# Performance work log

Hardware: AMD Instinct MI355X
Metric: run time of the kernel (lower is better)

The kernel has to match this reference:

```python
import jax, jax.numpy as jnp
import numpy as np

B, T_MEL, T_TXT = 16, 2048, 1024
D_MODEL, D_ENC_M, D_ENC_T = 512, 512, 512
LN_EPS = 1e-5


def setup_inputs() -> dict:
    key = jax.random.key(0)
    ks = jax.random.split(key, 9)
    mel_encoding = jax.random.normal(ks[0], (B, T_MEL, D_ENC_M), dtype=jnp.float32)
    text_encoding = jax.random.normal(ks[1], (B, T_TXT, D_ENC_T), dtype=jnp.float32)
    mel_mask = jax.random.randint(ks[2], (B, T_MEL), 0, 2).astype(bool)
    mel_mask = mel_mask.at[:, 0].set(False)  # guarantee >=1 unmasked key per row
    src_mask = jax.random.randint(ks[3], (B, T_TXT), 0, 2).astype(bool)
    # Projection weights stored [in, out] (torch Linear does x @ W.T)
    sc = 1.0 / np.sqrt(D_ENC_M)
    Wq = jax.random.uniform(ks[4], (D_ENC_T, D_MODEL), jnp.float32, -sc, sc)
    Wk = jax.random.uniform(ks[5], (D_ENC_M, D_MODEL), jnp.float32, -sc, sc)
    Wv = jax.random.uniform(ks[6], (D_ENC_M, D_MODEL), jnp.float32, -sc, sc)
    ln_gamma = jnp.ones((D_MODEL,), jnp.float32)
    ln_beta = jnp.zeros((D_MODEL,), jnp.float32)
    return {"mel_encoding": mel_encoding, "text_encoding": text_encoding,
            "mel_mask": mel_mask, "src_mask": src_mask,
            "Wq": Wq, "Wk": Wk, "Wv": Wv,
            "ln_gamma": ln_gamma, "ln_beta": ln_beta}


def reference(mel_encoding, text_encoding, mel_mask, src_mask, Wq, Wk, Wv, ln_gamma, ln_beta):
    temperature = jnp.sqrt(jnp.float32(D_ENC_M))
    q = jnp.einsum('btd,dm->btm', text_encoding, Wq)   # [B, T_txt, d_model]
    k = jnp.einsum('bsd,dm->bsm', mel_encoding, Wk)    # [B, T_mel, d_model]
    v = jnp.einsum('bsd,dm->bsm', mel_encoding, Wv)
    # attn_mask = outer product of src_mask and mel_mask (True -> masked)
    attn_mask = src_mask[:, :, None] & mel_mask[:, None, :]  # [B, T_txt, T_mel]
    scores = jnp.einsum('btm,bsm->bts', q, k) / temperature
    scores = jnp.where(attn_mask, -jnp.inf, scores)
    attn = jax.nn.softmax(scores, axis=2)
    output = jnp.einsum('bts,bsm->btm', attn, v)
    # dropout is identity at inference; LayerNorm over last dim
    mean = jnp.mean(output, axis=-1, keepdims=True)
    var = jnp.var(output, axis=-1, keepdims=True)
    output = (output - mean) * jax.lax.rsqrt(var + LN_EPS) * ln_gamma + ln_beta
    return output, attn
```

## Files before the change

kernel.cpp:

```cpp
#include <hip/hip_runtime.h>

#define DEV __device__ __forceinline__

typedef __attribute__((ext_vector_type(8))) short short8v;
typedef __attribute__((ext_vector_type(4))) float f32x4;

DEV unsigned short f2bf(float f) {
  unsigned int x = __float_as_uint(f);
  x = x + 0x7FFFu + ((x >> 16) & 1u);
  return (unsigned short)(x >> 16);
}
DEV float bf2f(unsigned short u) {
  return __uint_as_float(((unsigned)u) << 16);
}

DEV int swz_byte(int row, int kElem) {
  int chunk = ((kElem >> 3) ^ (row & 7));
  return row * 128 + (chunk << 4) + ((kElem & 7) << 1);
}

template <int ROUNDS>
DEV void stage(const unsigned short* __restrict__ g, int ld,
               unsigned short* tile, int tid) {
  const int wave = tid >> 6, l = tid & 63;
#pragma unroll
  for (int p = 0; p < ROUNDS; ++p) {
    const int r = (p << 5) + (wave << 3) + (l >> 3);
    const int c = ((l & 7) ^ (r & 7)) << 3;
    const unsigned short* src = g + (long)r * ld + c;
#if __has_builtin(__builtin_amdgcn_global_load_lds)
    unsigned short* dst = tile + (p << 11) + (wave << 9);
    __builtin_amdgcn_global_load_lds(
        (const __attribute__((address_space(1))) void*)src,
        (__attribute__((address_space(3))) void*)dst, 16, 0, 0);
#else
    short8v v = *reinterpret_cast<const short8v*>(src);
    *reinterpret_cast<short8v*>(reinterpret_cast<char*>(tile) +
                                (p << 12) + (wave << 10) + (l << 4)) = v;
#endif
  }
}

template <int BM>
DEV void stage_f32(const float* __restrict__ g, int ld,
                   unsigned short* tile, int tid) {
  const int rl = tid >> 4;
  const int c4 = (tid & 15) << 2;
#pragma unroll
  for (int p = 0; p < BM / 16; ++p) {
    const int row = (p << 4) + rl;
    const float4 f = *reinterpret_cast<const float4*>(g + (long)row * ld + c4);
    ushort4 pack;
    pack.x = f2bf(f.x); pack.y = f2bf(f.y); pack.z = f2bf(f.z); pack.w = f2bf(f.w);
    *reinterpret_cast<ushort4*>(reinterpret_cast<char*>(tile) +
                                swz_byte(row, c4)) = pack;
  }
}

template <int BM, int EPI, int GM, bool AF32>
__global__ __launch_bounds__(256) void gemm_bf16(
    const void* __restrict__ Av, const unsigned short* __restrict__ B,
    void* __restrict__ Cout, int M, int N, int K,
    long aBatch, long bBatch, long cBatch,
    const int* __restrict__ srcMask, const int* __restrict__ melMask,
    float scale, float* __restrict__ stats) {
  constexpr int NI = BM / 32;
  __shared__ unsigned short As[BM * 64];
  __shared__ unsigned short Bs[128 * 64];
  const int tid = threadIdx.x;
  const int lane = tid & 63;
  const int wave = tid >> 6;
  int z, bmi, bni;
  if constexpr (GM == 1) {
    const int id = blockIdx.x;
    z = (id & 7) | ((id >> 10) << 3);
    const int ib = (id >> 3) & 127;
    bni = ib & 15;
    bmi = ib >> 4;
  } else if constexpr (GM == 2) {
    bmi = blockIdx.x; bni = blockIdx.y; z = blockIdx.z;
  } else {
    bni = blockIdx.x; bmi = blockIdx.y; z = blockIdx.z;
  }
  const int bm = bmi * BM;
  const int bn = bni * 128;
  const unsigned short* Bb = B + (long)z * bBatch;
  const long cOff = (long)z * cBatch;
  const int wr = (wave >> 1) * (BM / 2);
  const int wc = (wave & 1) * 64;
  const int l15 = lane & 15;
  const int lHi = lane >> 4;

  f32x4 acc[NI][4] = {};

  for (int kt = 0; kt < K; kt += 64) {
    if constexpr (AF32) {
      stage_f32<BM>((const float*)Av + (long)z * aBatch + (long)bm * K + kt, K, As, tid);
    } else {
      stage<BM / 32>((const unsigned short*)Av + (long)z * aBatch + (long)bm * K + kt,
                     K, As, tid);
    }
    stage<4>(Bb + (long)bn * K + kt, K, Bs, tid);
    __syncthreads();
#pragma unroll
    for (int ks = 0; ks < 2; ++ks) {
      const int k0 = (ks << 5) + (lHi << 3);
      short8v af[NI], bfr[4];
#pragma unroll
      for (int i = 0; i < NI; ++i)
        af[i] = *reinterpret_cast<const short8v*>(
            reinterpret_cast<const char*>(As) + swz_byte(wr + i * 16 + l15, k0));
#pragma unroll
      for (int j = 0; j < 4; ++j)
        bfr[j] = *reinterpret_cast<const short8v*>(
            reinterpret_cast<const char*>(Bs) + swz_byte(wc + j * 16 + l15, k0));
#pragma unroll
      for (int i = 0; i < NI; ++i)
#pragma unroll
        for (int j = 0; j < 4; ++j)
          acc[i][j] = __builtin_amdgcn_mfma_f32_16x16x32_bf16(af[i], bfr[j], acc[i][j], 0, 0, 0);
    }
    __syncthreads();
  }

  if constexpr (EPI == 2) {
    const int wcIdx = wave & 1;
#pragma unroll
    for (int i = 0; i < NI; ++i) {
#pragma unroll
      for (int rr = 0; rr < 4; ++rr) {
        const int rloc = wr + i * 16 + lHi * 4 + rr;
        const int rb = bm + rloc;
        const bool sm = srcMask[z * 1024 + rb] != 0;
        float vals[4];
        float m_l = -3.0e38f;
#pragma unroll
        for (int j = 0; j < 4; ++j) {
          const int c = bn + wc + j * 16 + l15;
          const bool mm = melMask[z * 2048 + c] != 0;
          const float vf = (sm && mm) ? -1e30f : acc[i][j][rr] * scale;
          vals[j] = vf;
          m_l = fmaxf(m_l, vf);
        }
#pragma unroll
        for (int o = 1; o < 16; o <<= 1) m_l = fmaxf(m_l, __shfl_xor(m_l, o, 64));
        float s_l = 0.f;
#pragma unroll
        for (int j = 0; j < 4; ++j) {
          const float pe = __expf(vals[j] - m_l);
          s_l += pe;
          const int c = bn + wc + j * 16 + l15;
          reinterpret_cast<unsigned short*>(Cout)[cOff + (long)rb * N + c] = f2bf(pe);
        }
#pragma unroll
        for (int o = 1; o < 16; o <<= 1) s_l += __shfl_xor(s_l, o, 64);
        if (l15 == 0) {
          const long sidx = ((long)(z * 1024 + rb)) * 64 + (long)(bni * 2 + wcIdx) * 2;
          stats[sidx] = m_l;
          stats[sidx + 1] = s_l;
        }
      }
    }
  } else {
#pragma unroll
    for (int i = 0; i < NI; ++i) {
#pragma unroll
      for (int j = 0; j < 4; ++j) {
        const int rb = bm + wr + i * 16 + lHi * 4;
        const int c = bn + wc + j * 16 + l15;
#pragma unroll
        for (int r = 0; r < 4; ++r) {
          const long idx = cOff + (long)(rb + r) * N + c;
          reinterpret_cast<unsigned short*>(Cout)[idx] = f2bf(acc[i][j][r]);
        }
      }
    }
  }
}

__global__ __launch_bounds__(256) void pv_smx(
    const unsigned short* __restrict__ sbf, const unsigned short* __restrict__ vT,
    float* __restrict__ attn, float* __restrict__ out,
    const float* __restrict__ stats) {
  __shared__ unsigned short As[2][64 * 64];
  __shared__ unsigned short Bs[2][128 * 64];
  __shared__ unsigned short scl[64][34];
  const int id = blockIdx.x;
  const int z = (id & 7) | ((id >> 9) << 3);
  const int ib = (id >> 3) & 63;
  const int mt = ib & 15, nt = ib >> 4;
  const int bm = mt * 64, bn = nt * 128;
  const int tid = threadIdx.x, lane = tid & 63, wave = tid >> 6;

  {
    const int row = tid >> 2;
    const float* st = stats + ((long)(z * 1024 + bm + row)) * 64;
    float Mx = -3.0e38f;
#pragma unroll
    for (int t = 0; t < 32; ++t) Mx = fmaxf(Mx, st[t * 2]);
    float S = 0.f;
#pragma unroll
    for (int t = 0; t < 32; ++t) S += st[t * 2 + 1] * __expf(st[t * 2] - Mx);
    const float inv = 1.0f / S;
    const int t0 = (tid & 3) * 8;
#pragma unroll
    for (int t = 0; t < 8; ++t)
      scl[row][t0 + t] = f2bf(__expf(st[(t0 + t) * 2] - Mx) * inv);
  }
  __syncthreads();

  const int ar = tid >> 2;
  const int ac = (tid & 3) << 4;
  const long aOff = ((long)z * 1024 + bm + ar) * 2048 + ac;
  const unsigned short* vTb = vT + ((long)z * 512 + bn) * 2048;
  const int wr = (wave >> 1) * 32, wc = (wave & 1) * 64;
  const int l15 = lane & 15, lHi = lane >> 4;

  f32x4 acc[2][4] = {};

  for (int it = 0; it < 16; ++it) {
    const int kt = it << 7;
    stage<4>(vTb + kt, 2048, Bs[0], tid);
    stage<4>(vTb + kt + 64, 2048, Bs[1], tid);
#pragma unroll
    for (int h = 0; h < 2; ++h) {
      const int kh = kt + (h << 6);
      const float sc = bf2f(scl[ar][kh >> 6]);
      const short8v s0 = *reinterpret_cast<const short8v*>(sbf + aOff + kh);
      const short8v s1 = *reinterpret_cast<const short8v*>(sbf + aOff + kh + 8);
      float e[16];
#pragma unroll
      for (int u = 0; u < 8; ++u) {
        e[u] = bf2f((unsigned short)s0[u]) * sc;
        e[u + 8] = bf2f((unsigned short)s1[u]) * sc;
      }
      if ((kh >> 9) == nt) {
        float* ap = attn + aOff + kh;
#pragma unroll
        for (int g = 0; g < 4; ++g) {
          float4 w;
          w.x = e[g * 4]; w.y = e[g * 4 + 1]; w.z = e[g * 4 + 2]; w.w = e[g * 4 + 3];
          *reinterpret_cast<float4*>(ap + g * 4) = w;
        }
      }
      short8v pk0, pk1;
#pragma unroll
      for (int u = 0; u < 8; ++u) {
        pk0[u] = (short)f2bf(e[u]);
        pk1[u] = (short)f2bf(e[u + 8]);
      }
      *reinterpret_cast<short8v*>(reinterpret_cast<char*>(As[h]) + swz_byte(ar, ac)) = pk0;
      *reinterpret_cast<short8v*>(reinterpret_cast<char*>(As[h]) + swz_byte(ar, ac + 8)) = pk1;
    }
    __syncthreads();

#pragma unroll
    for (int h = 0; h < 2; ++h) {
#pragma unroll
      for (int ks = 0; ks < 2; ++ks) {
        const int k0 = (ks << 5) + (lHi << 3);
        short8v af[2], bfr[4];
#pragma unroll
        for (int i = 0; i < 2; ++i)
          af[i] = *reinterpret_cast<const short8v*>(
              reinterpret_cast<const char*>(As[h]) + swz_byte(wr + i * 16 + l15, k0));
#pragma unroll
        for (int j = 0; j < 4; ++j)
          bfr[j] = *reinterpret_cast<const short8v*>(
              reinterpret_cast<const char*>(Bs[h]) + swz_byte(wc + j * 16 + l15, k0));
#pragma unroll
        for (int i = 0; i < 2; ++i)
#pragma unroll
          for (int j = 0; j < 4; ++j)
            acc[i][j] = __builtin_amdgcn_mfma_f32_16x16x32_bf16(af[i], bfr[j], acc[i][j], 0, 0, 0);
      }
    }
    __syncthreads();
  }

#pragma unroll
  for (int i = 0; i < 2; ++i)
#pragma unroll
    for (int j = 0; j < 4; ++j) {
      const int row = bm + wr + i * 16 + lHi * 4;
      const int col = bn + wc + j * 16 + l15;
#pragma unroll
      for (int rr = 0; rr < 4; ++rr)
        out[((long)z * 1024 + row + rr) * 512 + col] = acc[i][j][rr];
    }
}

__global__ __launch_bounds__(256) void f32_to_bf16(
    const float* __restrict__ in, unsigned short* __restrict__ out, long n) {
  long i = ((long)blockIdx.x * blockDim.x + threadIdx.x) * 8;
  const long stride = (long)gridDim.x * blockDim.x * 8;
  for (; i < n; i += stride) {
    const float4 a = *reinterpret_cast<const float4*>(in + i);
    const float4 b = *reinterpret_cast<const float4*>(in + i + 4);
    short8v o;
    o[0] = (short)f2bf(a.x); o[1] = (short)f2bf(a.y);
    o[2] = (short)f2bf(a.z); o[3] = (short)f2bf(a.w);
    o[4] = (short)f2bf(b.x); o[5] = (short)f2bf(b.y);
    o[6] = (short)f2bf(b.z); o[7] = (short)f2bf(b.w);
    *reinterpret_cast<short8v*>(out + i) = o;
  }
}

__global__ __launch_bounds__(256) void prep_w(
    const float* __restrict__ Wq, const float* __restrict__ Wk,
    const float* __restrict__ Wv, unsigned short* __restrict__ wqbf,
    unsigned short* __restrict__ wkbf, unsigned short* __restrict__ WvT) {
  const int zz = blockIdx.z;
  const int tx = threadIdx.x, ty = threadIdx.y;
  if (zz == 0) {
    __shared__ float t[32][33];
    const int bx = blockIdx.x * 32;
    const int by = blockIdx.y * 32;
#pragma unroll
    for (int i = 0; i < 4; ++i)
      t[ty + i * 8][tx] = Wv[(long)(by + ty + i * 8) * 512 + bx + tx];
    __syncthreads();
#pragma unroll
    for (int i = 0; i < 4; ++i)
      WvT[(long)(bx + ty + i * 8) * 512 + by + tx] = f2bf(t[tx][ty + i * 8]);
  } else {
    const float* in = (zz == 1) ? Wq : Wk;
    unsigned short* out = (zz == 1) ? wqbf : wkbf;
    const long base = ((long)(blockIdx.y * 16 + blockIdx.x) * 256 + ty * 32 + tx) * 4;
    const float4 f = *reinterpret_cast<const float4*>(in + base);
    ushort4 o;
    o.x = f2bf(f.x); o.y = f2bf(f.y); o.z = f2bf(f.z); o.w = f2bf(f.w);
    *reinterpret_cast<ushort4*>(out + base) = o;
  }
}

__global__ __launch_bounds__(64) void layernorm_rows(
    float* __restrict__ out, const float* __restrict__ gamma, const float* __restrict__ beta) {
  const long row = blockIdx.x;
  float4* p = reinterpret_cast<float4*>(out + row * 512);
  const int lane = threadIdx.x;
  float4 a = p[lane];
  float4 b = p[lane + 64];
  float s = ((a.x + a.y) + (a.z + a.w)) + ((b.x + b.y) + (b.z + b.w));
  float s2 = ((a.x * a.x + a.y * a.y) + (a.z * a.z + a.w * a.w)) +
             ((b.x * b.x + b.y * b.y) + (b.z * b.z + b.w * b.w));
#pragma unroll
  for (int o = 32; o; o >>= 1) {
    s += __shfl_xor(s, o, 64);
    s2 += __shfl_xor(s2, o, 64);
  }
  const float mean = s * (1.0f / 512.0f);
  const float var = s2 * (1.0f / 512.0f) - mean * mean;
  const float rstd = rsqrtf(var + 1e-5f);
  const float4 g0 = reinterpret_cast<const float4*>(gamma)[lane];
  const float4 g1 = reinterpret_cast<const float4*>(gamma)[lane + 64];
  const float4 c0 = reinterpret_cast<const float4*>(beta)[lane];
  const float4 c1 = reinterpret_cast<const float4*>(beta)[lane + 64];
  a.x = (a.x - mean) * rstd * g0.x + c0.x;
  a.y = (a.y - mean) * rstd * g0.y + c0.y;
  a.z = (a.z - mean) * rstd * g0.z + c0.z;
  a.w = (a.w - mean) * rstd * g0.w + c0.w;
  b.x = (b.x - mean) * rstd * g1.x + c1.x;
  b.y = (b.y - mean) * rstd * g1.y + c1.y;
  b.z = (b.z - mean) * rstd * g1.z + c1.z;
  b.w = (b.w - mean) * rstd * g1.w + c1.w;
  p[lane] = a;
  p[lane + 64] = b;
}

extern "C" void kernel_launch(void* const* d_in, const int* in_sizes, int n_in,
                              void* d_out, int out_size, void* d_ws, size_t ws_size,
                              hipStream_t stream) {
  const float* mel  = (const float*)d_in[0];
  const float* text = (const float*)d_in[1];
  const int* melMask = (const int*)d_in[2];
  const int* srcMask = (const int*)d_in[3];
  const float* Wq = (const float*)d_in[4];
  const float* Wk = (const float*)d_in[5];
  const float* Wv = (const float*)d_in[6];
  const float* gamma = (const float*)d_in[7];
  const float* beta  = (const float*)d_in[8];

  float* out = (float*)d_out;
  float* attn = (float*)d_out + (long)16 * 1024 * 512;

  unsigned short* ws = (unsigned short*)d_ws;
  unsigned short* wqbf = ws;
  unsigned short* wkbf = wqbf + 512 * 512;
  unsigned short* wvT  = wkbf + 512 * 512;
  unsigned short* Mt   = wvT + 512 * 512;
  unsigned short* melbf = Mt + 512 * 512;
  unsigned short* qbf  = melbf + (long)16 * 2048 * 512;
  unsigned short* vT   = qbf + (long)16 * 1024 * 512;
  unsigned short* sbf  = vT + (long)16 * 512 * 2048;
  float* stats = (float*)(sbf + (long)16 * 1024 * 2048);

  prep_w<<<dim3(16, 16, 3), dim3(32, 8), 0, stream>>>(Wq, Wk, Wv, wqbf, wkbf, wvT);
  f32_to_bf16<<<dim3(4096), 256, 0, stream>>>(mel, melbf, (long)16 * 2048 * 512);

  gemm_bf16<128, 0, 0, false><<<dim3(4, 4, 1), 256, 0, stream>>>(
      wkbf, wqbf, Mt, 512, 512, 512, 0, 0, 0, nullptr, nullptr, 1.0f, nullptr);
  gemm_bf16<128, 0, 2, true><<<dim3(128, 4, 1), 256, 0, stream>>>(
      text, Mt, qbf, 16384, 512, 512, 0, 0, 0, nullptr, nullptr, 1.0f, nullptr);
  gemm_bf16<128, 0, 0, false><<<dim3(16, 4, 16), 256, 0, stream>>>(
      wvT, melbf, vT, 512, 2048, 512, 0, (long)2048 * 512, (long)512 * 2048,
      nullptr, nullptr, 1.0f, nullptr);
  gemm_bf16<128, 2, 1, false><<<dim3(2048), 256, 0, stream>>>(
      qbf, melbf, sbf, 1024, 2048, 512,
      (long)1024 * 512, (long)2048 * 512, (long)1024 * 2048,
      srcMask, melMask, 0.044194173824159216f, stats);
  pv_smx<<<dim3(1024), 256, 0, stream>>>(sbf, vT, attn, out, stats);
  layernorm_rows<<<dim3(16 * 1024), 64, 0, stream>>>(out, gamma, beta);
}
```

Measured before the change: 260.8 us.

## Merge independent launches into interleaved horizontally fused kernels

Moves the GEMM body into a device function and builds two combined kernels. One pairs the mel f32-to-bf16 conversion with the Q projection GEMM, and the other pairs the V-transpose GEMM with the scores GEMM, splitting block IDs by a fixed ratio. The aim is to save launch gaps and let memory-bound and compute-bound work share the GPU at the same time. The cost is that both halves of each combined kernel must use the same shared-memory size and register budget.

```diff
diff --git a/kernel.cpp b/kernel.cpp
--- a/kernel.cpp
+++ b/kernel.cpp
@@ -57,31 +57,18 @@
   }
 }
 
-template <int BM, int EPI, int GM, bool AF32>
-__global__ __launch_bounds__(256) void gemm_bf16(
-    const void* __restrict__ Av, const unsigned short* __restrict__ B,
-    void* __restrict__ Cout, int M, int N, int K,
-    long aBatch, long bBatch, long cBatch,
-    const int* __restrict__ srcMask, const int* __restrict__ melMask,
-    float scale, float* __restrict__ stats) {
+template <int BM, int EPI, bool AF32>
+DEV void gemm_body(const void* __restrict__ Av, const unsigned short* __restrict__ B,
+                   void* __restrict__ Cout, int M, int N, int K,
+                   long aBatch, long bBatch, long cBatch,
+                   const int* __restrict__ srcMask, const int* __restrict__ melMask,
+                   float scale, float* __restrict__ stats,
+                   int z, int bmi, int bni,
+                   unsigned short* As, unsigned short* Bs) {
   constexpr int NI = BM / 32;
-  __shared__ unsigned short As[BM * 64];
-  __shared__ unsigned short Bs[128 * 64];
   const int tid = threadIdx.x;
   const int lane = tid & 63;
   const int wave = tid >> 6;
-  int z, bmi, bni;
-  if constexpr (GM == 1) {
-    const int id = blockIdx.x;
-    z = (id & 7) | ((id >> 10) << 3);
-    const int ib = (id >> 3) & 127;
-    bni = ib & 15;
-    bmi = ib >> 4;
-  } else if constexpr (GM == 2) {
-    bmi = blockIdx.x; bni = blockIdx.y; z = blockIdx.z;
-  } else {
-    bni = blockIdx.x; bmi = blockIdx.y; z = blockIdx.z;
-  }
   const int bm = bmi * BM;
   const int bn = bni * 128;
   const unsigned short* Bb = B + (long)z * bBatch;
@@ -175,6 +162,75 @@
         }
       }
     }
+  }
+}
+
+template <int BM, int EPI, bool AF32>
+__global__ __launch_bounds__(256) void gemm_bf16(
+    const void* __restrict__ Av, const unsigned short* __restrict__ B,
+    void* __restrict__ Cout, int M, int N, int K,
+    long aBatch, long bBatch, long cBatch,
+    const int* __restrict__ srcMask, const int* __restrict__ melMask,
+    float scale, float* __restrict__ stats) {
+  __shared__ unsigned short As[BM * 64];
+  __shared__ unsigned short Bs[128 * 64];
+  gemm_body<BM, EPI, AF32>(Av, B, Cout, M, N, K, aBatch, bBatch, cBatch,
+                           srcMask, melMask, scale, stats,
+                           blockIdx.z, blockIdx.y, blockIdx.x, As, Bs);
+}
+
+__global__ __launch_bounds__(256) void fused_conv_q(
+    const float* __restrict__ mel, unsigned short* __restrict__ melbf,
+    const float* __restrict__ text, const unsigned short* __restrict__ Mt,
+    unsigned short* __restrict__ qbf) {
+  __shared__ unsigned short As[128 * 64];
+  __shared__ unsigned short Bs[128 * 64];
+  const int id = blockIdx.x;
+  const int a = id / 9, b = id - a * 9;
+  if (b == 8) {
+    gemm_body<128, 0, true>(text, Mt, qbf, 16384, 512, 512, 0, 0, 0,
+                            nullptr, nullptr, 1.0f, nullptr,
+                            0, a & 127, a >> 7, As, Bs);
+  } else {
+    const int cid = 8 * a + b;
+    long i = ((long)cid * 256 + threadIdx.x) * 8;
+    const long stride = 4096L * 256 * 8;
+    const long n = 16L * 2048 * 512;
+    for (; i < n; i += stride) {
+      const float4 x = *reinterpret_cast<const float4*>(mel + i);
+      const float4 y = *reinterpret_cast<const float4*>(mel + i + 4);
+      short8v o;
+      o[0] = (short)f2bf(x.x); o[1] = (short)f2bf(x.y);
+      o[2] = (short)f2bf(x.z); o[3] = (short)f2bf(x.w);
+      o[4] = (short)f2bf(y.x); o[5] = (short)f2bf(y.y);
+      o[6] = (short)f2bf(y.z); o[7] = (short)f2bf(y.w);
+      *reinterpret_cast<short8v*>(melbf + i) = o;
+    }
+  }
+}
+
+__global__ __launch_bounds__(256) void fused_sc_vt(
+    const unsigned short* __restrict__ qbf, const unsigned short* __restrict__ melbf,
+    unsigned short* __restrict__ sbf, float* __restrict__ stats,
+    const unsigned short* __restrict__ wvT, unsigned short* __restrict__ vT,
+    const int* __restrict__ srcMask, const int* __restrict__ melMask) {
+  __shared__ unsigned short As[128 * 64];
+  __shared__ unsigned short Bs[128 * 64];
+  const int id = blockIdx.x;
+  const int a = id / 3, b = id - a * 3;
+  if (b == 2) {
+    gemm_body<128, 0, false>(wvT, melbf, vT, 512, 2048, 512,
+                             0, (long)2048 * 512, (long)512 * 2048,
+                             nullptr, nullptr, 1.0f, nullptr,
+                             a >> 6, (a >> 4) & 3, a & 15, As, Bs);
+  } else {
+    const int cid = 2 * a + b;
+    const int z = (cid & 7) | ((cid >> 10) << 3);
+    const int ib = (cid >> 3) & 127;
+    gemm_body<128, 2, false>(qbf, melbf, sbf, 1024, 2048, 512,
+                             (long)1024 * 512, (long)2048 * 512, (long)1024 * 2048,
+                             srcMask, melMask, 0.044194173824159216f, stats,
+                             z, ib >> 4, ib & 15, As, Bs);
   }
 }
 
@@ -288,22 +344,6 @@
       for (int rr = 0; rr < 4; ++rr)
         out[((long)z * 1024 + row + rr) * 512 + col] = acc[i][j][rr];
     }
-}
-
-__global__ __launch_bounds__(256) void f32_to_bf16(
-    const float* __restrict__ in, unsigned short* __restrict__ out, long n) {
-  long i = ((long)blockIdx.x * blockDim.x + threadIdx.x) * 8;
-  const long stride = (long)gridDim.x * blockDim.x * 8;
-  for (; i < n; i += stride) {
-    const float4 a = *reinterpret_cast<const float4*>(in + i);
-    const float4 b = *reinterpret_cast<const float4*>(in + i + 4);
-    short8v o;
-    o[0] = (short)f2bf(a.x); o[1] = (short)f2bf(a.y);
-    o[2] = (short)f2bf(a.z); o[3] = (short)f2bf(a.w);
-    o[4] = (short)f2bf(b.x); o[5] = (short)f2bf(b.y);
-    o[6] = (short)f2bf(b.z); o[7] = (short)f2bf(b.w);
-    *reinterpret_cast<short8v*>(out + i) = o;
-  }
 }
 
 __global__ __launch_bounds__(256) void prep_w(
@@ -396,19 +436,11 @@
   float* stats = (float*)(sbf + (long)16 * 1024 * 2048);
 
   prep_w<<<dim3(16, 16, 3), dim3(32, 8), 0, stream>>>(Wq, Wk, Wv, wqbf, wkbf, wvT);
-  f32_to_bf16<<<dim3(4096), 256, 0, stream>>>(mel, melbf, (long)16 * 2048 * 512);
-
-  gemm_bf16<128, 0, 0, false><<<dim3(4, 4, 1), 256, 0, stream>>>(
+  gemm_bf16<128, 0, false><<<dim3(4, 4, 1), 256, 0, stream>>>(
       wkbf, wqbf, Mt, 512, 512, 512, 0, 0, 0, nullptr, nullptr, 1.0f, nullptr);
-  gemm_bf16<128, 0, 2, true><<<dim3(128, 4, 1), 256, 0, stream>>>(
-      text, Mt, qbf, 16384, 512, 512, 0, 0, 0, nullptr, nullptr, 1.0f, nullptr);
-  gemm_bf16<128, 0, 0, false><<<dim3(16, 4, 16), 256, 0, stream>>>(
-      wvT, melbf, vT, 512, 2048, 512, 0, (long)2048 * 512, (long)512 * 2048,
-      nullptr, nullptr, 1.0f, nullptr);
-  gemm_bf16<128, 2, 1, false><<<dim3(2048), 256, 0, stream>>>(
-      qbf, melbf, sbf, 1024, 2048, 512,
-      (long)1024 * 512, (long)2048 * 512, (long)1024 * 2048,
-      srcMask, melMask, 0.044194173824159216f, stats);
+  fused_conv_q<<<dim3(4608), 256, 0, stream>>>(mel, melbf, text, Mt, qbf);
+  fused_sc_vt<<<dim3(3072), 256, 0, stream>>>(
+      qbf, melbf, sbf, stats, wvT, vT, srcMask, melMask);
   pv_smx<<<dim3(1024), 256, 0, stream>>>(sbf, vT, attn, out, stats);
   layernorm_rows<<<dim3(16 * 1024), 64, 0, stream>>>(out, gamma, beta);
 }
```

Result: slower. 279.6 us (+7.2%).

## Software-pipeline PV kernel with async global-to-LDS loads of score tiles

Applied to the files above, without the earlier changes.

Restructures the pv_smx main loop into a double-buffered pipeline over 64-wide K tiles. The next tile of bf16 scores and V^T is issued with global_load_lds directly into shared memory while the current tile is transformed (rescaled, written to attn, repacked to bf16 in place) and multiplied with MFMA. The goal is to hide global load latency behind compute and avoid staging scores through registers. The price is more barriers per iteration (32 iterations instead of 16), manual waitcnt handling, and an in-place swizzled rewrite of the LDS buffer that must be correctly ordered across waves.

```diff
diff --git a/kernel.cpp b/kernel.cpp
--- a/kernel.cpp
+++ b/kernel.cpp
@@ -182,8 +182,8 @@
     const unsigned short* __restrict__ sbf, const unsigned short* __restrict__ vT,
     float* __restrict__ attn, float* __restrict__ out,
     const float* __restrict__ stats) {
-  __shared__ unsigned short As[2][64 * 64];
   __shared__ unsigned short Bs[2][128 * 64];
+  __shared__ unsigned short Ar[2][64 * 64];
   __shared__ unsigned short scl[64][34];
   const int id = blockIdx.x;
   const int z = (id & 7) | ((id >> 9) << 3);
@@ -209,73 +209,105 @@
   }
   __syncthreads();
 
-  const int ar = tid >> 2;
-  const int ac = (tid & 3) << 4;
-  const long aOff = ((long)z * 1024 + bm + ar) * 2048 + ac;
   const unsigned short* vTb = vT + ((long)z * 512 + bn) * 2048;
   const int wr = (wave >> 1) * 32, wc = (wave & 1) * 64;
   const int l15 = lane & 15, lHi = lane >> 4;
+  const int trow = (wave << 4) + (lane >> 2);
+  const int tac = (lane & 3) << 4;
 
   f32x4 acc[2][4] = {};
 
-  for (int it = 0; it < 16; ++it) {
-    const int kt = it << 7;
-    stage<4>(vTb + kt, 2048, Bs[0], tid);
-    stage<4>(vTb + kt + 64, 2048, Bs[1], tid);
-#pragma unroll
-    for (int h = 0; h < 2; ++h) {
-      const int kh = kt + (h << 6);
-      const float sc = bf2f(scl[ar][kh >> 6]);
-      const short8v s0 = *reinterpret_cast<const short8v*>(sbf + aOff + kh);
-      const short8v s1 = *reinterpret_cast<const short8v*>(sbf + aOff + kh + 8);
-      float e[16];
-#pragma unroll
-      for (int u = 0; u < 8; ++u) {
-        e[u] = bf2f((unsigned short)s0[u]) * sc;
-        e[u + 8] = bf2f((unsigned short)s1[u]) * sc;
+  auto issueT = [&](int t) {
+    const int kt = t << 6;
+    stage<4>(vTb + kt, 2048, Bs[t & 1], tid);
+#pragma unroll
+    for (int p = 0; p < 2; ++p) {
+      const int gr = (wave << 4) + (p << 3) + (lane >> 3);
+      const unsigned short* src =
+          sbf + ((long)(z * 1024 + bm + gr)) * 2048 + kt + ((lane & 7) << 3);
+#if __has_builtin(__builtin_amdgcn_global_load_lds)
+      unsigned short* dst = Ar[t & 1] + (wave << 10) + (p << 9);
+      __builtin_amdgcn_global_load_lds(
+          (const __attribute__((address_space(1))) void*)src,
+          (__attribute__((address_space(3))) void*)dst, 16, 0, 0);
+#else
+      short8v v = *reinterpret_cast<const short8v*>(src);
+      *reinterpret_cast<short8v*>(Ar[t & 1] + (wave << 10) + (p << 9) + lane * 8) = v;
+#endif
+    }
+  };
+
+  auto transform = [&](int t) {
+    const int kt = t << 6;
+    unsigned short* buf = Ar[t & 1];
+    const char* rb = reinterpret_cast<const char*>(buf) + (wave << 11) +
+                     (lane >> 2) * 128 + ((lane & 3) << 5);
+    const short8v r0 = *reinterpret_cast<const short8v*>(rb);
+    const short8v r1 = *reinterpret_cast<const short8v*>(rb + 16);
+    const float sc = bf2f(scl[trow][t]);
+    float e[16];
+#pragma unroll
+    for (int u = 0; u < 8; ++u) {
+      e[u] = bf2f((unsigned short)r0[u]) * sc;
+      e[u + 8] = bf2f((unsigned short)r1[u]) * sc;
+    }
+    if ((kt >> 9) == nt) {
+      float* ap = attn + ((long)(z * 1024 + bm + trow)) * 2048 + kt + tac;
+#pragma unroll
+      for (int g = 0; g < 4; ++g) {
+        float4 w;
+        w.x = e[g * 4]; w.y = e[g * 4 + 1]; w.z = e[g * 4 + 2]; w.w = e[g * 4 + 3];
+        *reinterpret_cast<float4*>(ap + g * 4) = w;
       }
-      if ((kh >> 9) == nt) {
-        float* ap = attn + aOff + kh;
-#pragma unroll
-        for (int g = 0; g < 4; ++g) {
-          float4 w;
-          w.x = e[g * 4]; w.y = e[g * 4 + 1]; w.z = e[g * 4 + 2]; w.w = e[g * 4 + 3];
-          *reinterpret_cast<float4*>(ap + g * 4) = w;
-        }
-      }
-      short8v pk0, pk1;
-#pragma unroll
-      for (int u = 0; u < 8; ++u) {
-        pk0[u] = (short)f2bf(e[u]);
-        pk1[u] = (short)f2bf(e[u + 8]);
-      }
-      *reinterpret_cast<short8v*>(reinterpret_cast<char*>(As[h]) + swz_byte(ar, ac)) = pk0;
-      *reinterpret_cast<short8v*>(reinterpret_cast<char*>(As[h]) + swz_byte(ar, ac + 8)) = pk1;
-    }
-    __syncthreads();
-
-#pragma unroll
-    for (int h = 0; h < 2; ++h) {
-#pragma unroll
-      for (int ks = 0; ks < 2; ++ks) {
-        const int k0 = (ks << 5) + (lHi << 3);
-        short8v af[2], bfr[4];
-#pragma unroll
-        for (int i = 0; i < 2; ++i)
-          af[i] = *reinterpret_cast<const short8v*>(
-              reinterpret_cast<const char*>(As[h]) + swz_byte(wr + i * 16 + l15, k0));
+    }
+    short8v pk0, pk1;
+#pragma unroll
+    for (int u = 0; u < 8; ++u) {
+      pk0[u] = (short)f2bf(e[u]);
+      pk1[u] = (short)f2bf(e[u + 8]);
+    }
+    *reinterpret_cast<short8v*>(reinterpret_cast<char*>(buf) + swz_byte(trow, tac)) = pk0;
+    *reinterpret_cast<short8v*>(reinterpret_cast<char*>(buf) + swz_byte(trow, tac + 8)) = pk1;
+  };
+
+  auto mfma_step = [&](int t) {
+    const unsigned short* aRd = Ar[t & 1];
+    const unsigned short* bRd = Bs[t & 1];
+#pragma unroll
+    for (int ks = 0; ks < 2; ++ks) {
+      const int k0 = (ks << 5) + (lHi << 3);
+      short8v af[2], bfr[4];
+#pragma unroll
+      for (int i = 0; i < 2; ++i)
+        af[i] = *reinterpret_cast<const short8v*>(
+            reinterpret_cast<const char*>(aRd) + swz_byte(wr + i * 16 + l15, k0));
+#pragma unroll
+      for (int j = 0; j < 4; ++j)
+        bfr[j] = *reinterpret_cast<const short8v*>(
+            reinterpret_cast<const char*>(bRd) + swz_byte(wc + j * 16 + l15, k0));
+#pragma unroll
+      for (int i = 0; i < 2; ++i)
 #pragma unroll
         for (int j = 0; j < 4; ++j)
-          bfr[j] = *reinterpret_cast<const short8v*>(
-              reinterpret_cast<const char*>(Bs[h]) + swz_byte(wc + j * 16 + l15, k0));
-#pragma unroll
-        for (int i = 0; i < 2; ++i)
-#pragma unroll
-          for (int j = 0; j < 4; ++j)
-            acc[i][j] = __builtin_amdgcn_mfma_f32_16x16x32_bf16(af[i], bfr[j], acc[i][j], 0, 0, 0);
-      }
-    }
-    __syncthreads();
+          acc[i][j] = __builtin_amdgcn_mfma_f32_16x16x32_bf16(af[i], bfr[j], acc[i][j], 0, 0, 0);
+    }
+  };
+
+  issueT(0);
+  asm volatile("s_waitcnt vmcnt(0)" ::: "memory");
+  __builtin_amdgcn_s_barrier();
+  __builtin_amdgcn_sched_barrier(0);
+
+  for (int t = 0; t < 32; ++t) {
+    if (t < 31) issueT(t + 1);
+    transform(t);
+    asm volatile("s_waitcnt lgkmcnt(0)" ::: "memory");
+    __builtin_amdgcn_s_barrier();
+    __builtin_amdgcn_sched_barrier(0);
+    mfma_step(t);
+    asm volatile("s_waitcnt vmcnt(0)" ::: "memory");
+    __builtin_amdgcn_s_barrier();
+    __builtin_amdgcn_sched_barrier(0);
   }
 
 #pragma unroll
```

Result: slower. 277.6 us (+6.4%).
